# Kernel optimization log

Measured on AMD Instinct MI355X. Metric: run time of the kernel, lower is better.

The kernel has to match this reference:

```python
import jax, jax.numpy as jnp
import numpy as np

IN_FEATURES = 128
OUT_FEATURES = 128
CAPACITY = 200000


def setup_inputs() -> dict:
    key = jax.random.key(0)
    k1, k2, k3 = jax.random.split(key, 3)
    query = jax.random.normal(k1, (IN_FEATURES,), dtype=jnp.float32)
    keys = jax.random.normal(k2, (CAPACITY, IN_FEATURES), dtype=jnp.float32)
    values = jax.random.normal(k3, (CAPACITY, OUT_FEATURES), dtype=jnp.float32)
    return {"query": query, "keys": keys, "values": values}


def reference(query, keys, values):
    # Negative L1 distance from query to each stored key: [N]
    diffs = -jnp.sum(jnp.abs(keys - query[None, :]), axis=1)
    # Softmax attention over all stored entries
    attention = jax.nn.softmax(diffs, axis=0)
    # Weighted sum of values: [out_features]
    out = attention @ values
    return out
```

## Files before the change

### kernel.cpp

```cpp
#include <hip/hip_runtime.h>
#include <math.h>

#define DIM 128
#define PSTRIDE 132
#define NEG_BIG (-3.0e38f)
#define THRESH 20.0f

__global__ __launch_bounds__(256) void nd_logits(const float* __restrict__ query,
                                                 const float* __restrict__ keys,
                                                 float* __restrict__ logits,
                                                 float* __restrict__ wsmax,
                                                 int nrows, int nchunks, int P) {
    const int tid  = threadIdx.x;
    const int lane = tid & 63;
    const int quad = lane & 3;
    const int rsub = lane >> 2;
    const int wid  = blockIdx.x * (blockDim.x >> 6) + (tid >> 6);

    float4 qv[8];
    #pragma unroll
    for (int j = 0; j < 8; ++j)
        qv[j] = *reinterpret_cast<const float4*>(query + quad * 4 + j * 16);

    const int q  = nchunks / P, r = nchunks % P;
    const int c0 = wid * q + (wid < r ? wid : r);
    const int c1 = c0 + q + (wid < r ? 1 : 0);

    float wmax = NEG_BIG;

    #define LBODY(cc)                                                             \
        {                                                                         \
            const int  row = (cc) * 16 + rsub;                                    \
            const bool ok  = row < nrows;                                         \
            const int  rr  = ok ? row : (nrows - 1);                              \
            const float* kp = keys + (size_t)rr * DIM + quad * 4;                 \
            float s = 0.f;                                                        \
            _Pragma("unroll")                                                     \
            for (int j = 0; j < 8; ++j) {                                         \
                const float4 k = *reinterpret_cast<const float4*>(kp + j * 16);   \
                s += fabsf(k.x - qv[j].x) + fabsf(k.y - qv[j].y)                  \
                   + fabsf(k.z - qv[j].z) + fabsf(k.w - qv[j].w);                 \
            }                                                                     \
            s += __shfl_xor(s, 1, 64);                                            \
            s += __shfl_xor(s, 2, 64);                                            \
            const float lg = ok ? -s : NEG_BIG;                                   \
            wmax = fmaxf(wmax, lg);                                               \
            if (quad == 0 && ok) logits[row] = lg;                                \
        }

    int c = c0;
    for (; c + 1 < c1; c += 2) { LBODY(c) LBODY(c + 1) }
    if (c < c1) LBODY(c)
    #undef LBODY

    #pragma unroll
    for (int off = 4; off < 64; off <<= 1)
        wmax = fmaxf(wmax, __shfl_xor(wmax, off, 64));
    if (lane == 0) wsmax[wid] = wmax;
}

__global__ __launch_bounds__(256) void nd_maxred(const float* __restrict__ wsmax,
                                                 float* __restrict__ maxval, int P) {
    __shared__ float sh[4];
    const int tid = threadIdx.x;
    float m = NEG_BIG;
    for (int i = tid; i < P; i += 256) m = fmaxf(m, wsmax[i]);
    #pragma unroll
    for (int off = 1; off < 64; off <<= 1)
        m = fmaxf(m, __shfl_xor(m, off, 64));
    if ((tid & 63) == 0) sh[tid >> 6] = m;
    __syncthreads();
    if (tid == 0)
        maxval[0] = fmaxf(fmaxf(sh[0], sh[1]), fmaxf(sh[2], sh[3]));
}

__global__ __launch_bounds__(256) void nd_accum(const float* __restrict__ values,
                                                const float* __restrict__ logits,
                                                const float* __restrict__ maxval,
                                                float* __restrict__ part,
                                                int nrows, int NW) {
    const int tid  = threadIdx.x;
    const int lane = tid & 63;
    const int wid  = blockIdx.x * (blockDim.x >> 6) + (tid >> 6);
    const float M  = maxval[0];
    const float cut = M - THRESH;

    float  l = 0.f;
    float2 acc = make_float2(0.f, 0.f);

    for (int base = wid * 64; base < nrows; base += NW * 64) {
        const int  row   = base + lane;
        const bool valid = row < nrows;
        const float lg   = valid ? logits[row] : NEG_BIG;
        const float w    = __expf(lg - M);
        l += w;
        unsigned long long ball = __ballot(valid && lg >= cut);
        while (ball) {
            const int b1 = __builtin_ctzll(ball); ball &= ball - 1;
            int b2 = -1;
            if (ball) { b2 = __builtin_ctzll(ball); ball &= ball - 1; }
            const float  w1 = __shfl(w, b1, 64);
            const float2 v1 = *reinterpret_cast<const float2*>(
                                  values + (size_t)(base + b1) * DIM + lane * 2);
            float  w2 = 0.f;
            float2 v2 = make_float2(0.f, 0.f);
            if (b2 >= 0) {
                w2 = __shfl(w, b2, 64);
                v2 = *reinterpret_cast<const float2*>(
                         values + (size_t)(base + b2) * DIM + lane * 2);
            }
            acc.x += w1 * v1.x + w2 * v2.x;
            acc.y += w1 * v1.y + w2 * v2.y;
        }
    }

    #pragma unroll
    for (int off = 1; off < 64; off <<= 1)
        l += __shfl_xor(l, off, 64);

    float* wp = part + (size_t)wid * PSTRIDE;
    if (lane == 0) wp[0] = l;
    *reinterpret_cast<float2*>(wp + 4 + lane * 2) = acc;
}

__global__ __launch_bounds__(256) void nd_merge(const float* __restrict__ part,
                                                float* __restrict__ part2) {
    __shared__ float sh_red[256];
    __shared__ float shL;
    const int tid  = threadIdx.x;
    const int base = blockIdx.x * 64;

    if (tid < 64) {
        float lp = part[(size_t)(base + tid) * PSTRIDE];
        #pragma unroll
        for (int off = 32; off > 0; off >>= 1)
            lp += __shfl_xor(lp, off, 64);
        if (tid == 0) shL = lp;
    }

    const int d = tid & 127, g = tid >> 7;
    float o = 0.f;
    for (int p = g; p < 64; p += 2)
        o += part[(size_t)(base + p) * PSTRIDE + 4 + d];
    sh_red[tid] = o;
    __syncthreads();

    if (tid < 128) {
        float* wp = part2 + (size_t)blockIdx.x * PSTRIDE;
        if (tid == 0) wp[0] = shL;
        wp[4 + tid] = sh_red[tid] + sh_red[tid + 128];
    }
}

__global__ __launch_bounds__(256) void nd_final(const float* __restrict__ part2,
                                                float* __restrict__ out, int B2) {
    __shared__ float sh_red[256];
    __shared__ float shL;
    const int tid = threadIdx.x;

    if (tid < 64) {
        float lp = 0.f;
        for (int p = tid; p < B2; p += 64)
            lp += part2[(size_t)p * PSTRIDE];
        #pragma unroll
        for (int off = 32; off > 0; off >>= 1)
            lp += __shfl_xor(lp, off, 64);
        if (tid == 0) shL = lp;
    }

    const int d = tid & 127, g = tid >> 7;
    float o = 0.f;
    for (int p = g; p < B2; p += 2)
        o += part2[(size_t)p * PSTRIDE + 4 + d];
    sh_red[tid] = o;
    __syncthreads();

    if (tid < 128)
        out[tid] = (sh_red[tid] + sh_red[tid + 128]) / shL;
}

extern "C" void kernel_launch(void* const* d_in, const int* in_sizes, int n_in,
                              void* d_out, int out_size, void* d_ws, size_t ws_size,
                              hipStream_t stream) {
    const float* query  = (const float*)d_in[0];
    const float* keys   = (const float*)d_in[1];
    const float* values = (const float*)d_in[2];
    float* out = (float*)d_out;
    float* ws  = (float*)d_ws;

    const int nrows   = in_sizes[1] / DIM;
    const int nchunks = (nrows + 15) / 16;
    const int LN      = (nrows + 63) & ~63;

    int P  = 4096;
    int NW = 4096;
    const size_t capf = ws_size / sizeof(float);
    while ((size_t)LN + (size_t)P + 16
           + (size_t)(NW + NW / 64) * PSTRIDE > capf && P > 512) {
        P >>= 1; NW >>= 1;
    }
    const int B2 = NW / 64;

    float* logits = ws;
    float* wsmax  = ws + LN;
    float* maxval = wsmax + P;
    float* part   = maxval + 16;
    float* part2  = part + (size_t)NW * PSTRIDE;

    nd_logits<<<P / 4, 256, 0, stream>>>(query, keys, logits, wsmax, nrows, nchunks, P);
    nd_maxred<<<1,     256, 0, stream>>>(wsmax, maxval, P);
    nd_accum <<<NW / 4, 256, 0, stream>>>(values, logits, maxval, part, nrows, NW);
    nd_merge <<<B2,    256, 0, stream>>>(part, part2);
    nd_final <<<1,     256, 0, stream>>>(part2, out, B2);
}
```

Baseline: 50.38 us.

## Fold max reduction into accumulate kernel and spread logits over two chunks per wave

```diff
diff --git a/kernel.cpp b/kernel.cpp
--- a/kernel.cpp
+++ b/kernel.cpp
@@ -6,11 +6,11 @@
 #define NEG_BIG (-3.0e38f)
 #define THRESH 20.0f
 
-__global__ __launch_bounds__(256) void nd_logits(const float* __restrict__ query,
-                                                 const float* __restrict__ keys,
-                                                 float* __restrict__ logits,
-                                                 float* __restrict__ wsmax,
-                                                 int nrows, int nchunks, int P) {
+__global__ __launch_bounds__(256, 2) void nd_logits(const float* __restrict__ query,
+                                                    const float* __restrict__ keys,
+                                                    float* __restrict__ logits,
+                                                    float* __restrict__ wsmax,
+                                                    int nrows, int nchunks, int P) {
     const int tid  = threadIdx.x;
     const int lane = tid & 63;
     const int quad = lane & 3;
@@ -34,13 +34,15 @@
             const bool ok  = row < nrows;                                         \
             const int  rr  = ok ? row : (nrows - 1);                              \
             const float* kp = keys + (size_t)rr * DIM + quad * 4;                 \
+            float4 kv[8];                                                         \
+            _Pragma("unroll")                                                     \
+            for (int j = 0; j < 8; ++j)                                           \
+                kv[j] = *reinterpret_cast<const float4*>(kp + j * 16);            \
             float s = 0.f;                                                        \
             _Pragma("unroll")                                                     \
-            for (int j = 0; j < 8; ++j) {                                         \
-                const float4 k = *reinterpret_cast<const float4*>(kp + j * 16);   \
-                s += fabsf(k.x - qv[j].x) + fabsf(k.y - qv[j].y)                  \
-                   + fabsf(k.z - qv[j].z) + fabsf(k.w - qv[j].w);                 \
-            }                                                                     \
+            for (int j = 0; j < 8; ++j)                                           \
+                s += fabsf(kv[j].x - qv[j].x) + fabsf(kv[j].y - qv[j].y)          \
+                   + fabsf(kv[j].z - qv[j].z) + fabsf(kv[j].w - qv[j].w);         \
             s += __shfl_xor(s, 1, 64);                                            \
             s += __shfl_xor(s, 2, 64);                                            \
             const float lg = ok ? -s : NEG_BIG;                                   \
@@ -59,30 +61,27 @@
     if (lane == 0) wsmax[wid] = wmax;
 }
 
-__global__ __launch_bounds__(256) void nd_maxred(const float* __restrict__ wsmax,
-                                                 float* __restrict__ maxval, int P) {
-    __shared__ float sh[4];
-    const int tid = threadIdx.x;
-    float m = NEG_BIG;
-    for (int i = tid; i < P; i += 256) m = fmaxf(m, wsmax[i]);
-    #pragma unroll
-    for (int off = 1; off < 64; off <<= 1)
-        m = fmaxf(m, __shfl_xor(m, off, 64));
-    if ((tid & 63) == 0) sh[tid >> 6] = m;
-    __syncthreads();
-    if (tid == 0)
-        maxval[0] = fmaxf(fmaxf(sh[0], sh[1]), fmaxf(sh[2], sh[3]));
-}
-
 __global__ __launch_bounds__(256) void nd_accum(const float* __restrict__ values,
                                                 const float* __restrict__ logits,
-                                                const float* __restrict__ maxval,
+                                                const float* __restrict__ wsmax,
                                                 float* __restrict__ part,
-                                                int nrows, int NW) {
+                                                int nrows, int P, int NW) {
+    __shared__ float sh4[4];
+    __shared__ float shM;
     const int tid  = threadIdx.x;
     const int lane = tid & 63;
     const int wid  = blockIdx.x * (blockDim.x >> 6) + (tid >> 6);
-    const float M  = maxval[0];
+
+    float m = NEG_BIG;
+    for (int i = tid; i < P; i += 256) m = fmaxf(m, wsmax[i]);
+    #pragma unroll
+    for (int off = 1; off < 64; off <<= 1)
+        m = fmaxf(m, __shfl_xor(m, off, 64));
+    if ((tid & 63) == 0) sh4[tid >> 6] = m;
+    __syncthreads();
+    if (tid == 0) shM = fmaxf(fmaxf(sh4[0], sh4[1]), fmaxf(sh4[2], sh4[3]));
+    __syncthreads();
+    const float M   = shM;
     const float cut = M - THRESH;
 
     float  l = 0.f;
@@ -192,24 +191,23 @@
     const int nchunks = (nrows + 15) / 16;
     const int LN      = (nrows + 63) & ~63;
 
-    int P  = 4096;
+    int P = (((nchunks + 1) / 2) + 3) & ~3;
+    if (P < 256) P = 256;
+
     int NW = 4096;
     const size_t capf = ws_size / sizeof(float);
     while ((size_t)LN + (size_t)P + 16
-           + (size_t)(NW + NW / 64) * PSTRIDE > capf && P > 512) {
-        P >>= 1; NW >>= 1;
-    }
+           + (size_t)(NW + NW / 64) * PSTRIDE > capf && NW > 512)
+        NW >>= 1;
     const int B2 = NW / 64;
 
     float* logits = ws;
     float* wsmax  = ws + LN;
-    float* maxval = wsmax + P;
-    float* part   = maxval + 16;
+    float* part   = wsmax + ((P + 15) & ~15);
     float* part2  = part + (size_t)NW * PSTRIDE;
 
-    nd_logits<<<P / 4, 256, 0, stream>>>(query, keys, logits, wsmax, nrows, nchunks, P);
-    nd_maxred<<<1,     256, 0, stream>>>(wsmax, maxval, P);
-    nd_accum <<<NW / 4, 256, 0, stream>>>(values, logits, maxval, part, nrows, NW);
-    nd_merge <<<B2,    256, 0, stream>>>(part, part2);
-    nd_final <<<1,     256, 0, stream>>>(part2, out, B2);
-}
+    nd_logits<<<P / 4,  256, 0, stream>>>(query, keys, logits, wsmax, nrows, nchunks, P);
+    nd_accum <<<NW / 4, 256, 0, stream>>>(values, logits, wsmax, part, nrows, P, NW);
+    nd_merge <<<B2,     256, 0, stream>>>(part, part2);
+    nd_final <<<1,      256, 0, stream>>>(part2, out, B2);
+}
```

Result: faster. 48.80 us (-3.1%).
